# Performance work log

Hardware: AMD Instinct MI355X
Metric: run time of the kernel (lower is better)

The kernel has to match this reference:

```python
import jax, jax.numpy as jnp
import numpy as np

N_NODES = 100000
N_EDGES = 1200000
N_GRAPHS = 8
IN_DIM = 64
HID = 64
N_CLASSES = 2


def setup_inputs() -> dict:
    key = jax.random.key(0)
    ks = jax.random.split(key, 8)
    features = jax.random.normal(ks[0], (N_NODES, IN_DIM), dtype=jnp.float32)
    W1 = jax.random.normal(ks[1], (IN_DIM, HID), dtype=jnp.float32) * (1.0 / np.sqrt(IN_DIM))
    b1 = jnp.zeros((HID,), dtype=jnp.float32)
    W2 = jax.random.normal(ks[2], (HID, HID), dtype=jnp.float32) * (1.0 / np.sqrt(HID))
    b2 = jnp.zeros((HID,), dtype=jnp.float32)
    Wp = jax.random.normal(ks[3], (HID, N_CLASSES), dtype=jnp.float32) * (1.0 / np.sqrt(HID))
    bp = jnp.zeros((N_CLASSES,), dtype=jnp.float32)
    edge_src = jax.random.randint(ks[4], (N_EDGES,), 0, N_NODES, dtype=jnp.int64 if jax.config.jax_enable_x64 else jnp.int32)
    edge_dst = jax.random.randint(ks[5], (N_EDGES,), 0, N_NODES, dtype=edge_src.dtype)
    graph_id = jnp.sort(jax.random.randint(ks[6], (N_NODES,), 0, N_GRAPHS, dtype=edge_src.dtype))
    return {"features": features, "W1": W1, "b1": b1, "W2": W2, "b2": b2,
            "Wp": Wp, "bp": bp, "edge_src": edge_src, "edge_dst": edge_dst,
            "graph_id": graph_id}


def reference(features, W1, b1, W2, b2, Wp, bp, edge_src, edge_dst, graph_id):
    N = features.shape[0]
    dt = features.dtype
    ones_e = jnp.ones(edge_src.shape[0], dtype=dt)
    # DGL GraphConv norm='both': symmetric normalization with out-deg (src) / in-deg (dst)
    out_deg = jnp.clip(jax.ops.segment_sum(ones_e, edge_src, num_segments=N), 1.0)
    in_deg = jnp.clip(jax.ops.segment_sum(ones_e, edge_dst, num_segments=N), 1.0)
    src_norm = jax.lax.rsqrt(out_deg)[:, None]  # [N,1]
    dst_norm = jax.lax.rsqrt(in_deg)[:, None]   # [N,1]

    def gconv(h, W, b):
        h = h * src_norm
        msgs = h[edge_src]                                    # [E, d] gather
        agg = jax.ops.segment_sum(msgs, edge_dst, num_segments=N)  # [N, d]
        agg = agg * dst_norm
        return jax.nn.relu(agg @ W + b)

    h = gconv(features, W1, b1)   # [N, HID]
    h = gconv(h, W2, b2)          # [N, HID]

    # dgl.mean_nodes: per-graph mean pooling
    cnt = jnp.clip(jax.ops.segment_sum(jnp.ones(N, dtype=dt), graph_id, num_segments=N_GRAPHS), 1.0)
    hg = jax.ops.segment_sum(h, graph_id, num_segments=N_GRAPHS) / cnt[:, None]  # [G, HID]
    return hg @ Wp + bp
```

## Files before the change

kernel.cpp:

```cpp
#include <hip/hip_runtime.h>

#define NN 100000
#define NE 1200000
#define NG 8
#define DIM 64
#define WROW 64
#define SCAN_BS 256
#define NB ((NN + SCAN_BS - 1) / SCAN_BS)
#define COLCAP (NE + 7 * NN)

#define RANGE 8192
#define NR 13
#define GSL 28
#define SLICE4 ((NE / 4 + GSL - 1) / GSL)

__global__ __launch_bounds__(256) void hist_kernel(const int4* __restrict__ esrc4,
                                                   const int4* __restrict__ edst4,
                                                   int* __restrict__ partial) {
  __shared__ int h[RANGE];
  int job = blockIdx.x;
  int g = job % GSL;
  int r = (job / GSL) % NR;
  int dir = job / (GSL * NR);
  const int4* __restrict__ idx = dir ? edst4 : esrc4;
  int lo = r * RANGE, hi = min(lo + RANGE, NN);
  for (int i = threadIdx.x; i < RANGE / 4; i += 256) ((int4*)h)[i] = make_int4(0, 0, 0, 0);
  __syncthreads();
  int s0 = g * SLICE4, s1 = min(s0 + SLICE4, NE / 4);
  for (int i = s0 + threadIdx.x; i < s1; i += 256) {
    int4 v = idx[i];
    if (v.x >= lo && v.x < hi) atomicAdd(&h[v.x - lo], 1);
    if (v.y >= lo && v.y < hi) atomicAdd(&h[v.y - lo], 1);
    if (v.z >= lo && v.z < hi) atomicAdd(&h[v.z - lo], 1);
    if (v.w >= lo && v.w < hi) atomicAdd(&h[v.w - lo], 1);
  }
  __syncthreads();
  int4* dst = (int4*)(partial + (size_t)job * RANGE);
  int cap4 = (hi - lo) >> 2;
  for (int i = threadIdx.x; i < cap4; i += 256) dst[i] = ((int4*)h)[i];
}

__global__ void reduce_kernel(const int* __restrict__ partial, int* __restrict__ indeg,
                              float* __restrict__ snormA, float* __restrict__ dnormA, int N) {
  int t = blockIdx.x * blockDim.x + threadIdx.x;
  if (t >= 2 * N) return;
  int dir = t >= N;
  int n = dir ? t - N : t;
  int r = n >> 13, off = n & (RANGE - 1);
  const int* p = partial + (((size_t)dir * NR + r) * GSL) * RANGE + off;
  int s = 0;
#pragma unroll
  for (int g = 0; g < GSL; ++g) s += p[(size_t)g * RANGE];
  float nv = rsqrtf(fmaxf((float)s, 1.0f));
  if (dir) { indeg[n] = s; dnormA[n] = nv; }
  else snormA[n] = nv;
}

__global__ __launch_bounds__(SCAN_BS) void scan1_kernel(const int* __restrict__ indeg,
                                                        int* __restrict__ rp2,
                                                        int* __restrict__ bsum, int N) {
  __shared__ int t[SCAN_BS];
  int i = blockIdx.x * SCAN_BS + threadIdx.x;
  int v = (i < N) ? ((indeg[i] + 7) & ~7) : 0;
  t[threadIdx.x] = v;
  __syncthreads();
  for (int off = 1; off < SCAN_BS; off <<= 1) {
    int u = (threadIdx.x >= off) ? t[threadIdx.x - off] : 0;
    __syncthreads();
    t[threadIdx.x] += u;
    __syncthreads();
  }
  if (i < N) rp2[i] = t[threadIdx.x] - v;
  if (i == N - 1) rp2[N] = t[threadIdx.x];
  if (threadIdx.x == SCAN_BS - 1) bsum[blockIdx.x] = t[threadIdx.x];
}

__global__ __launch_bounds__(512) void scan2_kernel(const int* __restrict__ bsum,
                                                    int* __restrict__ boff, int nb) {
  __shared__ int t[512];
  int v = ((int)threadIdx.x < nb) ? bsum[threadIdx.x] : 0;
  t[threadIdx.x] = v;
  __syncthreads();
  for (int off = 1; off < 512; off <<= 1) {
    int u = (threadIdx.x >= off) ? t[threadIdx.x - off] : 0;
    __syncthreads();
    t[threadIdx.x] += u;
    __syncthreads();
  }
  boff[threadIdx.x] = t[threadIdx.x] - v;
}

__global__ __launch_bounds__(SCAN_BS) void scan3_kernel(int* __restrict__ rp2,
                                                        const int* __restrict__ boff, int N) {
  int i = blockIdx.x * SCAN_BS + threadIdx.x;
  if (i < N) rp2[i] += boff[blockIdx.x];
  if (i == N - 1) rp2[N] += boff[blockIdx.x];
}

__global__ void offscan_kernel(int* __restrict__ partial, const int* __restrict__ rp2, int N) {
  int n = blockIdx.x * blockDim.x + threadIdx.x;
  if (n >= N) return;
  int r = n >> 13, i = n & (RANGE - 1);
  int* p = partial + (((size_t)NR + r) * GSL) * RANGE + i;
  int running = rp2[n];
#pragma unroll
  for (int g = 0; g < GSL; ++g) {
    int tmp = p[(size_t)g * RANGE];
    p[(size_t)g * RANGE] = running;
    running += tmp;
  }
}

__global__ void colinit_kernel(int4* __restrict__ col4, int n4) {
  int i = blockIdx.x * blockDim.x + threadIdx.x;
  int st = gridDim.x * blockDim.x;
  for (; i < n4; i += st) col4[i] = make_int4(NN, NN, NN, NN);
}

__global__ __launch_bounds__(256) void fill_kernel(const int4* __restrict__ esrc4,
                                                   const int4* __restrict__ edst4,
                                                   const int* __restrict__ partial,
                                                   int* __restrict__ col) {
  __shared__ int cnt[RANGE];
  int job = blockIdx.x;
  int g = job % GSL, r = job / GSL;
  int lo = r * RANGE, hi = min(lo + RANGE, NN);
  const int* off = partial + (((size_t)NR + r) * GSL + g) * RANGE;
  for (int i = threadIdx.x; i < hi - lo; i += 256) cnt[i] = off[i];
  __syncthreads();
  int s0 = g * SLICE4, s1 = min(s0 + SLICE4, NE / 4);
  for (int i = s0 + threadIdx.x; i < s1; i += 256) {
    int4 d = edst4[i];
    int4 s = esrc4[i];
    if (d.x >= lo && d.x < hi) col[atomicAdd(&cnt[d.x - lo], 1)] = s.x;
    if (d.y >= lo && d.y < hi) col[atomicAdd(&cnt[d.y - lo], 1)] = s.y;
    if (d.z >= lo && d.z < hi) col[atomicAdd(&cnt[d.z - lo], 1)] = s.z;
    if (d.w >= lo && d.w < hi) col[atomicAdd(&cnt[d.w - lo], 1)] = s.w;
  }
}

__global__ void prescale_kernel(const float* __restrict__ f, const float* __restrict__ snormA,
                                float* __restrict__ xs, int N) {
  int i = blockIdx.x * blockDim.x + threadIdx.x;
  if (i < N * 16) {
    int n = i >> 4;
    float sn = snormA[n];
    float4 v = ((const float4*)f)[i];
    v.x *= sn; v.y *= sn; v.z *= sn; v.w *= sn;
    ((float4*)xs)[i] = v;
  }
}

template <int POOL>
__global__ __launch_bounds__(256) void gconv_kernel(
    const float* __restrict__ xs, const float* __restrict__ snormA, const float* __restrict__ dnormA,
    const int* __restrict__ rp2, const int* __restrict__ col,
    const float* __restrict__ W, const float* __restrict__ b,
    float* __restrict__ out, const int* __restrict__ gid,
    float* __restrict__ gsum, float* __restrict__ gcnt, int N) {
  __shared__ float Wt[DIM * WROW];
  __shared__ float aL[4][4][DIM];
  __shared__ float lsum[NG * DIM];
  __shared__ float lcnt[NG];
  for (int i = threadIdx.x; i < DIM * 16; i += 256) {
    int k = i >> 4, ch = i & 15;
    *(float4*)&Wt[k * WROW + ch * 4] = *(const float4*)(W + k * DIM + ch * 4);
  }
  if (POOL) {
    for (int i = threadIdx.x; i < NG * DIM; i += 256) lsum[i] = 0.0f;
    if (threadIdx.x < NG) lcnt[threadIdx.x] = 0.0f;
  }
  __syncthreads();

  const int lane = threadIdx.x & 63;
  const int wid = threadIdx.x >> 6;
  const int g = lane >> 4;
  const int idx = lane & 15;
  const int t4 = idx << 2;
  const float4 bb = *(const float4*)(b + t4);
  const int waveId = blockIdx.x * 4 + wid;
  const int stride4 = gridDim.x * 16;

  for (int n4 = waveId * 4; n4 < N; n4 += stride4) {
    int n = n4 + g;
    bool valid = n < N;
    int nc = valid ? n : 0;
    int base = rp2[nc];
    int end = rp2[nc + 1];
    float4 acc = make_float4(0.f, 0.f, 0.f, 0.f);
    float4 acc2 = make_float4(0.f, 0.f, 0.f, 0.f);
    for (int p = base; p < end; p += 8) {
      int4 c0 = *(const int4*)(col + p);
      int4 c1 = *(const int4*)(col + p + 4);
      float4 v0 = *(const float4*)(xs + (size_t)c0.x * DIM + t4);
      float4 v1 = *(const float4*)(xs + (size_t)c0.y * DIM + t4);
      float4 v2 = *(const float4*)(xs + (size_t)c0.z * DIM + t4);
      float4 v3 = *(const float4*)(xs + (size_t)c0.w * DIM + t4);
      float4 v4 = *(const float4*)(xs + (size_t)c1.x * DIM + t4);
      float4 v5 = *(const float4*)(xs + (size_t)c1.y * DIM + t4);
      float4 v6 = *(const float4*)(xs + (size_t)c1.z * DIM + t4);
      float4 v7 = *(const float4*)(xs + (size_t)c1.w * DIM + t4);
      acc.x += (v0.x + v1.x) + (v2.x + v3.x);
      acc.y += (v0.y + v1.y) + (v2.y + v3.y);
      acc.z += (v0.z + v1.z) + (v2.z + v3.z);
      acc.w += (v0.w + v1.w) + (v2.w + v3.w);
      acc2.x += (v4.x + v5.x) + (v6.x + v7.x);
      acc2.y += (v4.y + v5.y) + (v6.y + v7.y);
      acc2.z += (v4.z + v5.z) + (v6.z + v7.z);
      acc2.w += (v4.w + v5.w) + (v6.w + v7.w);
    }
    float dn = dnormA[nc];
    acc.x = (acc.x + acc2.x) * dn;
    acc.y = (acc.y + acc2.y) * dn;
    acc.z = (acc.z + acc2.z) * dn;
    acc.w = (acc.w + acc2.w) * dn;

    *(float4*)&aL[wid][g][t4] = acc;

    float4 r = bb;
#pragma unroll
    for (int kc = 0; kc < 16; ++kc) {
      float4 av = *(const float4*)&aL[wid][g][4 * kc];
      float4 w0 = *(const float4*)(Wt + (4 * kc + 0) * WROW + t4);
      float4 w1 = *(const float4*)(Wt + (4 * kc + 1) * WROW + t4);
      float4 w2 = *(const float4*)(Wt + (4 * kc + 2) * WROW + t4);
      float4 w3 = *(const float4*)(Wt + (4 * kc + 3) * WROW + t4);
      r.x = fmaf(av.x, w0.x, r.x); r.y = fmaf(av.x, w0.y, r.y);
      r.z = fmaf(av.x, w0.z, r.z); r.w = fmaf(av.x, w0.w, r.w);
      r.x = fmaf(av.y, w1.x, r.x); r.y = fmaf(av.y, w1.y, r.y);
      r.z = fmaf(av.y, w1.z, r.z); r.w = fmaf(av.y, w1.w, r.w);
      r.x = fmaf(av.z, w2.x, r.x); r.y = fmaf(av.z, w2.y, r.y);
      r.z = fmaf(av.z, w2.z, r.z); r.w = fmaf(av.z, w2.w, r.w);
      r.x = fmaf(av.w, w3.x, r.x); r.y = fmaf(av.w, w3.y, r.y);
      r.z = fmaf(av.w, w3.z, r.z); r.w = fmaf(av.w, w3.w, r.w);
    }
    r.x = fmaxf(r.x, 0.f); r.y = fmaxf(r.y, 0.f);
    r.z = fmaxf(r.z, 0.f); r.w = fmaxf(r.w, 0.f);

    if (POOL) {
      if (valid) {
        int gi = gid[n];
        atomicAdd(&lsum[gi * DIM + t4 + 0], r.x);
        atomicAdd(&lsum[gi * DIM + t4 + 1], r.y);
        atomicAdd(&lsum[gi * DIM + t4 + 2], r.z);
        atomicAdd(&lsum[gi * DIM + t4 + 3], r.w);
        if (idx == 0) atomicAdd(&lcnt[gi], 1.0f);
      }
    } else if (valid) {
      float sn = snormA[n];
      float4 o = make_float4(r.x * sn, r.y * sn, r.z * sn, r.w * sn);
      *(float4*)(out + (size_t)n * DIM + t4) = o;
    }
  }

  if (POOL) {
    __syncthreads();
    for (int i = threadIdx.x; i < NG * DIM; i += 256) atomicAdd(&gsum[i], lsum[i]);
    if (threadIdx.x < NG) atomicAdd(&gcnt[threadIdx.x], lcnt[threadIdx.x]);
  }
}

__global__ void final_kernel(const float* __restrict__ gsum, const float* __restrict__ gcnt,
                             const float* __restrict__ Wp, const float* __restrict__ bp,
                             float* __restrict__ out) {
  int lane = threadIdx.x;
#pragma unroll
  for (int g = 0; g < NG; ++g) {
    float inv = 1.0f / fmaxf(gcnt[g], 1.0f);
    float hv = gsum[g * DIM + lane] * inv;
#pragma unroll
    for (int c = 0; c < 2; ++c) {
      float p = hv * Wp[lane * 2 + c];
      for (int off = 32; off; off >>= 1) p += __shfl_down(p, off, 64);
      if (lane == 0) out[g * 2 + c] = p + bp[c];
    }
  }
}

extern "C" void kernel_launch(void* const* d_in, const int* in_sizes, int n_in,
                              void* d_out, int out_size, void* d_ws, size_t ws_size,
                              hipStream_t stream) {
  const float* features = (const float*)d_in[0];
  const float* W1 = (const float*)d_in[1];
  const float* b1 = (const float*)d_in[2];
  const float* W2 = (const float*)d_in[3];
  const float* b2 = (const float*)d_in[4];
  const float* Wp = (const float*)d_in[5];
  const float* bp = (const float*)d_in[6];
  const int* esrc = (const int*)d_in[7];
  const int* edst = (const int*)d_in[8];
  const int* gid = (const int*)d_in[9];
  float* out = (float*)d_out;

  const int N = NN;

  float* base = (float*)d_ws;
  size_t off = 0;
  auto alloc = [&](size_t nwords) { size_t r = off; off = (off + nwords + 15) & ~(size_t)15; return r; };

  float* gsum = base + alloc(NG * DIM);
  float* gcnt = base + alloc(NG);
  size_t zeroWords = off;
  int* indeg  = (int*)(base + alloc(N));
  float* snormA = base + alloc(N);
  float* dnormA = base + alloc(N);
  int* rp2   = (int*)(base + alloc(N + 1));
  int* bsum  = (int*)(base + alloc(512));
  int* boff  = (int*)(base + alloc(512));
  int* col   = (int*)(base + alloc(COLCAP));
  float* xs  = base + alloc((size_t)(N + 1) * DIM);
  float* B   = base + alloc((size_t)(N + 1) * DIM);
  int* partial = (int*)xs;

  hipMemsetAsync(d_ws, 0, zeroWords * sizeof(float), stream);
  hipMemsetAsync(xs + (size_t)N * DIM, 0, DIM * sizeof(float), stream);
  hipMemsetAsync(B + (size_t)N * DIM, 0, DIM * sizeof(float), stream);

  hist_kernel<<<2 * NR * GSL, 256, 0, stream>>>((const int4*)esrc, (const int4*)edst, partial);
  reduce_kernel<<<(2 * N + 255) / 256, 256, 0, stream>>>(partial, indeg, snormA, dnormA, N);

  scan1_kernel<<<NB, SCAN_BS, 0, stream>>>(indeg, rp2, bsum, N);
  scan2_kernel<<<1, 512, 0, stream>>>(bsum, boff, NB);
  scan3_kernel<<<NB, SCAN_BS, 0, stream>>>(rp2, boff, N);

  offscan_kernel<<<(NR * RANGE + 255) / 256, 256, 0, stream>>>(partial, rp2, N);
  colinit_kernel<<<(COLCAP / 4 + 255) / 256, 256, 0, stream>>>((int4*)col, COLCAP / 4);
  fill_kernel<<<NR * GSL, 256, 0, stream>>>((const int4*)esrc, (const int4*)edst, partial, col);

  prescale_kernel<<<(N * 16 + 255) / 256, 256, 0, stream>>>(features, snormA, xs, N);

  gconv_kernel<0><<<2048, 256, 0, stream>>>(xs, snormA, dnormA, rp2, col, W1, b1,
                                            B, gid, gsum, gcnt, N);
  gconv_kernel<1><<<2048, 256, 0, stream>>>(B, snormA, dnormA, rp2, col, W2, b2,
                                            nullptr, gid, gsum, gcnt, N);

  final_kernel<<<1, 64, 0, stream>>>(gsum, gcnt, Wp, bp, out);
}
```

Measured before the change: 247.3 us.

## Apply weight matmul before aggregation via separate tiled GEMM kernel

Uses linearity to reorder each graph conv: the dense feature transform X·W runs first in a new shared-memory-tiled GEMM kernel (fusing the source-norm prescale), and the gather kernel then only aggregates neighbor rows, applies the dest norm, bias and ReLU. This takes the per-node 64x64 matmul out of the latency-bound gather loop and removes the LDS round trip per node, and the gather kernel gets a higher occupancy hint. In exchange it adds an extra full read/write pass over the node features for each layer and changes the floating-point summation order.

```diff
diff --git a/kernel.cpp b/kernel.cpp
--- a/kernel.cpp
+++ b/kernel.cpp
@@ -4,10 +4,10 @@
 #define NE 1200000
 #define NG 8
 #define DIM 64
-#define WROW 64
 #define SCAN_BS 256
 #define NB ((NN + SCAN_BS - 1) / SCAN_BS)
 #define COLCAP (NE + 7 * NN)
+#define GT 128
 
 #define RANGE 8192
 #define NR 13
@@ -139,45 +139,91 @@
   }
 }
 
-__global__ void prescale_kernel(const float* __restrict__ f, const float* __restrict__ snormA,
-                                float* __restrict__ xs, int N) {
-  int i = blockIdx.x * blockDim.x + threadIdx.x;
-  if (i < N * 16) {
-    int n = i >> 4;
-    float sn = snormA[n];
-    float4 v = ((const float4*)f)[i];
-    v.x *= sn; v.y *= sn; v.z *= sn; v.w *= sn;
-    ((float4*)xs)[i] = v;
-  }
+template <int SCALE>
+__global__ __launch_bounds__(256) void gemm_kernel(
+    const float* __restrict__ X, const float* __restrict__ snormA,
+    const float* __restrict__ W, float* __restrict__ Z, int N) {
+  __shared__ float aT[DIM][GT + 1];
+  __shared__ float Wl[DIM][DIM + 4];
+  const int t = threadIdx.x;
+  const int nb = blockIdx.x * GT;
+
+  for (int i = t; i < DIM * 16; i += 256) {
+    int k = i >> 4, c4 = (i & 15) << 2;
+    *(float4*)&Wl[k][c4] = *(const float4*)(W + k * DIM + c4);
+  }
+#pragma unroll
+  for (int r = 0; r < 8; ++r) {
+    int i = t + r * 256;
+    int node = i >> 4, kc = i & 15;
+    int n = nb + node;
+    float4 a = make_float4(0.f, 0.f, 0.f, 0.f);
+    float sc = 1.0f;
+    if (n < N) {
+      a = *(const float4*)(X + (size_t)n * DIM + kc * 4);
+      if (SCALE) sc = snormA[n];
+    }
+    if (SCALE) { a.x *= sc; a.y *= sc; a.z *= sc; a.w *= sc; }
+    aT[kc * 4 + 0][node] = a.x;
+    aT[kc * 4 + 1][node] = a.y;
+    aT[kc * 4 + 2][node] = a.z;
+    aT[kc * 4 + 3][node] = a.w;
+  }
+  __syncthreads();
+
+  const int n0 = (t >> 4) * 8;
+  const int j0 = (t & 15) * 4;
+  float4 acc0 = {0,0,0,0}, acc1 = {0,0,0,0}, acc2 = {0,0,0,0}, acc3 = {0,0,0,0};
+  float4 acc4 = {0,0,0,0}, acc5 = {0,0,0,0}, acc6 = {0,0,0,0}, acc7 = {0,0,0,0};
+#pragma unroll 4
+  for (int k = 0; k < DIM; ++k) {
+    float4 w = *(const float4*)&Wl[k][j0];
+    float4 aA = *(const float4*)&aT[k][n0];
+    float4 aB = *(const float4*)&aT[k][n0 + 4];
+    acc0.x = fmaf(aA.x, w.x, acc0.x); acc0.y = fmaf(aA.x, w.y, acc0.y);
+    acc0.z = fmaf(aA.x, w.z, acc0.z); acc0.w = fmaf(aA.x, w.w, acc0.w);
+    acc1.x = fmaf(aA.y, w.x, acc1.x); acc1.y = fmaf(aA.y, w.y, acc1.y);
+    acc1.z = fmaf(aA.y, w.z, acc1.z); acc1.w = fmaf(aA.y, w.w, acc1.w);
+    acc2.x = fmaf(aA.z, w.x, acc2.x); acc2.y = fmaf(aA.z, w.y, acc2.y);
+    acc2.z = fmaf(aA.z, w.z, acc2.z); acc2.w = fmaf(aA.z, w.w, acc2.w);
+    acc3.x = fmaf(aA.w, w.x, acc3.x); acc3.y = fmaf(aA.w, w.y, acc3.y);
+    acc3.z = fmaf(aA.w, w.z, acc3.z); acc3.w = fmaf(aA.w, w.w, acc3.w);
+    acc4.x = fmaf(aB.x, w.x, acc4.x); acc4.y = fmaf(aB.x, w.y, acc4.y);
+    acc4.z = fmaf(aB.x, w.z, acc4.z); acc4.w = fmaf(aB.x, w.w, acc4.w);
+    acc5.x = fmaf(aB.y, w.x, acc5.x); acc5.y = fmaf(aB.y, w.y, acc5.y);
+    acc5.z = fmaf(aB.y, w.z, acc5.z); acc5.w = fmaf(aB.y, w.w, acc5.w);
+    acc6.x = fmaf(aB.z, w.x, acc6.x); acc6.y = fmaf(aB.z, w.y, acc6.y);
+    acc6.z = fmaf(aB.z, w.z, acc6.z); acc6.w = fmaf(aB.z, w.w, acc6.w);
+    acc7.x = fmaf(aB.w, w.x, acc7.x); acc7.y = fmaf(aB.w, w.y, acc7.y);
+    acc7.z = fmaf(aB.w, w.z, acc7.z); acc7.w = fmaf(aB.w, w.w, acc7.w);
+  }
+  int n = nb + n0;
+#define STORE_Z(m, accm) if (n + m < N) *(float4*)(Z + (size_t)(n + m) * DIM + j0) = accm;
+  STORE_Z(0, acc0) STORE_Z(1, acc1) STORE_Z(2, acc2) STORE_Z(3, acc3)
+  STORE_Z(4, acc4) STORE_Z(5, acc5) STORE_Z(6, acc6) STORE_Z(7, acc7)
+#undef STORE_Z
 }
 
 template <int POOL>
-__global__ __launch_bounds__(256) void gconv_kernel(
-    const float* __restrict__ xs, const float* __restrict__ snormA, const float* __restrict__ dnormA,
+__global__ __launch_bounds__(256, 8) void gather_kernel(
+    const float* __restrict__ xs, const float* __restrict__ dnormA,
+    const float* __restrict__ bias, const float* __restrict__ snormA,
     const int* __restrict__ rp2, const int* __restrict__ col,
-    const float* __restrict__ W, const float* __restrict__ b,
-    float* __restrict__ out, const int* __restrict__ gid,
+    float* __restrict__ y, const int* __restrict__ gid,
     float* __restrict__ gsum, float* __restrict__ gcnt, int N) {
-  __shared__ float Wt[DIM * WROW];
-  __shared__ float aL[4][4][DIM];
   __shared__ float lsum[NG * DIM];
   __shared__ float lcnt[NG];
-  for (int i = threadIdx.x; i < DIM * 16; i += 256) {
-    int k = i >> 4, ch = i & 15;
-    *(float4*)&Wt[k * WROW + ch * 4] = *(const float4*)(W + k * DIM + ch * 4);
-  }
   if (POOL) {
     for (int i = threadIdx.x; i < NG * DIM; i += 256) lsum[i] = 0.0f;
     if (threadIdx.x < NG) lcnt[threadIdx.x] = 0.0f;
-  }
-  __syncthreads();
-
+    __syncthreads();
+  }
   const int lane = threadIdx.x & 63;
   const int wid = threadIdx.x >> 6;
   const int g = lane >> 4;
   const int idx = lane & 15;
   const int t4 = idx << 2;
-  const float4 bb = *(const float4*)(b + t4);
+  const float4 bb = *(const float4*)(bias + t4);
   const int waveId = blockIdx.x * 4 + wid;
   const int stride4 = gridDim.x * 16;
 
@@ -209,47 +255,25 @@
       acc2.z += (v4.z + v5.z) + (v6.z + v7.z);
       acc2.w += (v4.w + v5.w) + (v6.w + v7.w);
     }
-    float dn = dnormA[nc];
-    acc.x = (acc.x + acc2.x) * dn;
-    acc.y = (acc.y + acc2.y) * dn;
-    acc.z = (acc.z + acc2.z) * dn;
-    acc.w = (acc.w + acc2.w) * dn;
-
-    *(float4*)&aL[wid][g][t4] = acc;
-
-    float4 r = bb;
-#pragma unroll
-    for (int kc = 0; kc < 16; ++kc) {
-      float4 av = *(const float4*)&aL[wid][g][4 * kc];
-      float4 w0 = *(const float4*)(Wt + (4 * kc + 0) * WROW + t4);
-      float4 w1 = *(const float4*)(Wt + (4 * kc + 1) * WROW + t4);
-      float4 w2 = *(const float4*)(Wt + (4 * kc + 2) * WROW + t4);
-      float4 w3 = *(const float4*)(Wt + (4 * kc + 3) * WROW + t4);
-      r.x = fmaf(av.x, w0.x, r.x); r.y = fmaf(av.x, w0.y, r.y);
-      r.z = fmaf(av.x, w0.z, r.z); r.w = fmaf(av.x, w0.w, r.w);
-      r.x = fmaf(av.y, w1.x, r.x); r.y = fmaf(av.y, w1.y, r.y);
-      r.z = fmaf(av.y, w1.z, r.z); r.w = fmaf(av.y, w1.w, r.w);
-      r.x = fmaf(av.z, w2.x, r.x); r.y = fmaf(av.z, w2.y, r.y);
-      r.z = fmaf(av.z, w2.z, r.z); r.w = fmaf(av.z, w2.w, r.w);
-      r.x = fmaf(av.w, w3.x, r.x); r.y = fmaf(av.w, w3.y, r.y);
-      r.z = fmaf(av.w, w3.z, r.z); r.w = fmaf(av.w, w3.w, r.w);
-    }
-    r.x = fmaxf(r.x, 0.f); r.y = fmaxf(r.y, 0.f);
-    r.z = fmaxf(r.z, 0.f); r.w = fmaxf(r.w, 0.f);
-
-    if (POOL) {
-      if (valid) {
+    if (valid) {
+      float dn = dnormA[n];
+      float4 r;
+      r.x = fmaxf(fmaf(dn, acc.x + acc2.x, bb.x), 0.f);
+      r.y = fmaxf(fmaf(dn, acc.y + acc2.y, bb.y), 0.f);
+      r.z = fmaxf(fmaf(dn, acc.z + acc2.z, bb.z), 0.f);
+      r.w = fmaxf(fmaf(dn, acc.w + acc2.w, bb.w), 0.f);
+      if (POOL) {
         int gi = gid[n];
         atomicAdd(&lsum[gi * DIM + t4 + 0], r.x);
         atomicAdd(&lsum[gi * DIM + t4 + 1], r.y);
         atomicAdd(&lsum[gi * DIM + t4 + 2], r.z);
         atomicAdd(&lsum[gi * DIM + t4 + 3], r.w);
         if (idx == 0) atomicAdd(&lcnt[gi], 1.0f);
+      } else {
+        float sn = snormA[n];
+        r.x *= sn; r.y *= sn; r.z *= sn; r.w *= sn;
+        *(float4*)(y + (size_t)n * DIM + t4) = r;
       }
-    } else if (valid) {
-      float sn = snormA[n];
-      float4 o = make_float4(r.x * sn, r.y * sn, r.z * sn, r.w * sn);
-      *(float4*)(out + (size_t)n * DIM + t4) = o;
     }
   }
 
@@ -314,7 +338,6 @@
 
   hipMemsetAsync(d_ws, 0, zeroWords * sizeof(float), stream);
   hipMemsetAsync(xs + (size_t)N * DIM, 0, DIM * sizeof(float), stream);
-  hipMemsetAsync(B + (size_t)N * DIM, 0, DIM * sizeof(float), stream);
 
   hist_kernel<<<2 * NR * GSL, 256, 0, stream>>>((const int4*)esrc, (const int4*)edst, partial);
   reduce_kernel<<<(2 * N + 255) / 256, 256, 0, stream>>>(partial, indeg, snormA, dnormA, N);
@@ -327,12 +350,13 @@
   colinit_kernel<<<(COLCAP / 4 + 255) / 256, 256, 0, stream>>>((int4*)col, COLCAP / 4);
   fill_kernel<<<NR * GSL, 256, 0, stream>>>((const int4*)esrc, (const int4*)edst, partial, col);
 
-  prescale_kernel<<<(N * 16 + 255) / 256, 256, 0, stream>>>(features, snormA, xs, N);
-
-  gconv_kernel<0><<<2048, 256, 0, stream>>>(xs, snormA, dnormA, rp2, col, W1, b1,
-                                            B, gid, gsum, gcnt, N);
-  gconv_kernel<1><<<2048, 256, 0, stream>>>(B, snormA, dnormA, rp2, col, W2, b2,
-                                            nullptr, gid, gsum, gcnt, N);
+  const int GB = (N + GT - 1) / GT;
+  gemm_kernel<1><<<GB, 256, 0, stream>>>(features, snormA, W1, xs, N);
+  gather_kernel<0><<<2048, 256, 0, stream>>>(xs, dnormA, b1, snormA, rp2, col,
+                                             B, gid, gsum, gcnt, N);
+  gemm_kernel<0><<<GB, 256, 0, stream>>>(B, snormA, W2, xs, N);
+  gather_kernel<1><<<2048, 256, 0, stream>>>(xs, dnormA, b2, snormA, rp2, col,
+                                             nullptr, gid, gsum, gcnt, N);
 
   final_kernel<<<1, 64, 0, stream>>>(gsum, gcnt, Wp, bp, out);
 }
```

Result: slower. 269.6 us (+9.0%).
